# Kernel tuning notes

Measured on AMD Instinct MI355X. Metric: run time of the kernel, lower is better.

Reference implementation:

```python
import jax, jax.numpy as jnp
import numpy as np

B, H, W, C = 8, 64, 64, 256
CB = C // 2          # bottleneck_dim = channels // 2
COMPRESSION = 2      # max-pool factor on flattened spatial axis of phi and g


def setup_inputs() -> dict:
    key = jax.random.key(0)
    k = jax.random.split(key, 5)
    he = lambda kk, fan_in, shape: jax.random.normal(kk, shape, jnp.float32) * np.sqrt(2.0 / fan_in)
    return {
        "x": jax.random.normal(k[0], (B, H, W, C), jnp.float32),
        "W_theta": he(k[1], C, (C, CB)),
        "W_phi": he(k[2], C, (C, CB)),
        "W_g": he(k[3], C, (C, CB)),
        "W_out": he(k[4], CB, (CB, C)),
    }


def _maxpool1d(t, pool):
    # MaxPool1D(pool) along axis 1 of [B, N, C] (valid padding, stride=pool)
    b, n, c = t.shape
    return t.reshape(b, n // pool, pool, c).max(axis=2)


def reference(x, W_theta, W_phi, W_g, W_out):
    b, h, w, c = x.shape
    n = h * w
    xf = x.reshape(b, n, c)                      # flatten spatial dims
    theta = xf @ W_theta                         # [B, N, Cb] (1x1 conv, no bias)
    phi = _maxpool1d(xf @ W_phi, COMPRESSION)    # [B, N/2, Cb]
    g = _maxpool1d(xf @ W_g, COMPRESSION)        # [B, N/2, Cb]
    f = jax.nn.softmax(jnp.einsum('bnd,bmd->bnm', theta, phi), axis=-1)  # [B, N, N/2]
    y = jnp.einsum('bnm,bmd->bnd', f, g)         # [B, N, Cb]
    y = (y @ W_out).reshape(b, h, w, c)          # expand conv back to C
    return x + y                                 # add_residual=True
```

## Files before the change

### kernel.cpp

```cpp
#include <hip/hip_runtime.h>
#include <math.h>

#define BB 8
#define NN 4096
#define MM 2048
#define CC 256
#define CBD 128

typedef __attribute__((ext_vector_type(8))) short s16x8;
typedef __attribute__((ext_vector_type(4))) float f32x4;
typedef __attribute__((ext_vector_type(16))) float f32x16;
typedef unsigned short u16;
typedef unsigned int u32;

__device__ __forceinline__ u16 f2bf(float f) {
    union { float f; u32 u; } v; v.f = f;
    u32 r = v.u + 0x7fffu + ((v.u >> 16) & 1u);
    return (u16)(r >> 16);
}
__device__ __forceinline__ float bf2f(u16 h) {
    union { u32 u; float f; } v; v.u = ((u32)h) << 16; return v.f;
}
__device__ __forceinline__ u32 asu(float f) {
    union { float f; u32 u; } v; v.f = f; return v.u;
}
__device__ __forceinline__ u32 pkbf(float lo, float hi) {
    return __builtin_amdgcn_perm(asu(hi), asu(lo), 0x07060302u);
}

#define MFMA(a, b, c)   __builtin_amdgcn_mfma_f32_16x16x32_bf16(a, b, c, 0, 0, 0)
#define MFMA32(a, b, c) __builtin_amdgcn_mfma_f32_32x32x16_bf16(a, b, c, 0, 0, 0)

__device__ __forceinline__ void gload_lds16(const u16* g, u16* l) {
    __builtin_amdgcn_global_load_lds(
        (const __attribute__((address_space(1))) void*)g,
        (__attribute__((address_space(3))) void*)l, 16, 0, 0);
}

__global__ __launch_bounds__(256) void k_split_w(
    const float* __restrict__ wt, const float* __restrict__ wp,
    const float* __restrict__ wg, const float* __restrict__ wo,
    u16* wth, u16* wtl, u16* wph, u16* wpl, u16* wgh, u16* wgl, u16* wot) {
    int e = blockIdx.x * 256 + threadIdx.x;
    int m = blockIdx.y;
    if (m < 3) {
        const float* src = m == 0 ? wt : (m == 1 ? wp : wg);
        u16* oh = m == 0 ? wth : (m == 1 ? wph : wgh);
        u16* ol = m == 0 ? wtl : (m == 1 ? wpl : wgl);
        int r = e >> 7, c = e & 127;
        float f = src[e];
        u16 hi = f2bf(f);
        oh[c * 256 + r] = hi;
        ol[c * 256 + r] = f2bf(f - bf2f(hi));
    } else {
        int r = e >> 8, c = e & 255;
        wot[c * 128 + r] = f2bf(wo[e]);
    }
}

__global__ __launch_bounds__(256) void k_proj(
    const float* __restrict__ x,
    const u16* __restrict__ wth, const u16* __restrict__ wtl,
    const u16* __restrict__ wph, const u16* __restrict__ wpl,
    const u16* __restrict__ wgh,
    u16* __restrict__ th, u16* __restrict__ tl,
    u16* __restrict__ ph, u16* __restrict__ pl, u16* __restrict__ gt) {
    __shared__ u16 S[31232];
    const int THH = 0, THL = 8704, PHH = 17408, PHL = 21760, GL = 26112;
    u16* sxh = S;
    u16* sxl = S + 2560;
    u16* sw  = S + 5120;
    int tid = threadIdx.x;
    int w = tid >> 6, lane = tid & 63, q = lane >> 4, li = lane & 15;
    int r0 = blockIdx.x * 64;
    int wr2 = (w >> 1) * 32, wcc = (w & 1) * 64;
    const u16* Ws[5] = {wth, wtl, wph, wpl, wgh};

    f32x4 aT[2][4], aP[2][4], aG[2][4];
#pragma unroll
    for (int i = 0; i < 2; i++)
#pragma unroll
        for (int j = 0; j < 4; j++) {
            aT[i][j] = (f32x4)0.f; aP[i][j] = (f32x4)0.f; aG[i][j] = (f32x4)0.f;
        }

    for (int kc = 0; kc < 8; kc++) {
        {
            int row = tid >> 2, seg = tid & 3;
            const float* xp = &x[(size_t)(r0 + row) * 256 + kc * 32 + seg * 8];
            float4 v0 = ((const float4*)xp)[0];
            float4 v1 = ((const float4*)xp)[1];
            float vv[8] = {v0.x, v0.y, v0.z, v0.w, v1.x, v1.y, v1.z, v1.w};
            u16 hh[8], ll[8];
#pragma unroll
            for (int t = 0; t < 8; t++) {
                hh[t] = f2bf(vv[t]);
                ll[t] = f2bf(vv[t] - bf2f(hh[t]));
            }
            *(s16x8*)&sxh[row * 40 + seg * 8] = *(s16x8*)&hh[0];
            *(s16x8*)&sxl[row * 40 + seg * 8] = *(s16x8*)&ll[0];
        }
#pragma unroll
        for (int u = 0; u < 10; u++) {
            int mat = u >> 1;
            int col = (u & 1) * 64 + (tid >> 2), ch = tid & 3;
            s16x8 v = *(const s16x8*)&Ws[mat][(size_t)col * 256 + kc * 32 + ch * 8];
            *(s16x8*)&sw[mat * 5120 + col * 40 + ch * 8] = v;
        }
        __syncthreads();

        s16x8 ah[2], al[2];
#pragma unroll
        for (int i = 0; i < 2; i++) {
            ah[i] = *(const s16x8*)&sxh[(wr2 + i * 16 + li) * 40 + q * 8];
            al[i] = *(const s16x8*)&sxl[(wr2 + i * 16 + li) * 40 + q * 8];
        }
#pragma unroll
        for (int j = 0; j < 4; j++) {
            int col = wcc + j * 16 + li;
            s16x8 bth = *(const s16x8*)&sw[0 * 5120 + col * 40 + q * 8];
            s16x8 btl = *(const s16x8*)&sw[1 * 5120 + col * 40 + q * 8];
            s16x8 bph = *(const s16x8*)&sw[2 * 5120 + col * 40 + q * 8];
            s16x8 bpl = *(const s16x8*)&sw[3 * 5120 + col * 40 + q * 8];
            s16x8 bgh = *(const s16x8*)&sw[4 * 5120 + col * 40 + q * 8];
#pragma unroll
            for (int i = 0; i < 2; i++) {
                aT[i][j] = MFMA(ah[i], bth, aT[i][j]);
                aT[i][j] = MFMA(al[i], bth, aT[i][j]);
                aT[i][j] = MFMA(ah[i], btl, aT[i][j]);
                aP[i][j] = MFMA(ah[i], bph, aP[i][j]);
                aP[i][j] = MFMA(al[i], bph, aP[i][j]);
                aP[i][j] = MFMA(ah[i], bpl, aP[i][j]);
                aG[i][j] = MFMA(ah[i], bgh, aG[i][j]);
                aG[i][j] = MFMA(al[i], bgh, aG[i][j]);
            }
        }
        __syncthreads();
    }

#pragma unroll
    for (int i = 0; i < 2; i++)
#pragma unroll
        for (int j = 0; j < 4; j++) {
            int col = wcc + j * 16 + li;
#pragma unroll
            for (int reg = 0; reg < 4; reg++) {
                int row = wr2 + i * 16 + q * 4 + reg;
                float v = aT[i][j][reg];
                u16 hi = f2bf(v);
                S[THH + row * 136 + col] = hi;
                S[THL + row * 136 + col] = f2bf(v - bf2f(hi));
            }
#pragma unroll
            for (int pr = 0; pr < 2; pr++) {
                int ml = (wr2 >> 1) + i * 8 + q * 2 + pr;
                float vp = fmaxf(aP[i][j][pr * 2], aP[i][j][pr * 2 + 1]);
                u16 hi = f2bf(vp);
                S[PHH + ml * 136 + col] = hi;
                S[PHL + ml * 136 + col] = f2bf(vp - bf2f(hi));
                float vg = fmaxf(aG[i][j][pr * 2], aG[i][j][pr * 2 + 1]);
                int ml2 = (ml & ~12) | ((ml & 4) << 1) | ((ml & 8) >> 1);
                S[GL + col * 40 + ml2] = f2bf(vg);
            }
        }
    __syncthreads();

#pragma unroll
    for (int p2 = 0; p2 < 4; p2++) {
        int u2 = tid + p2 * 256;
        int row = u2 >> 4, chk = u2 & 15;
        size_t gb = (size_t)(r0 + row) * 128 + chk * 8;
        *(s16x8*)&th[gb] = *(const s16x8*)&S[THH + row * 136 + chk * 8];
        *(s16x8*)&tl[gb] = *(const s16x8*)&S[THL + row * 136 + chk * 8];
    }
    {
        int row = tid >> 3, chk = tid & 7;
        size_t gb = (size_t)((r0 >> 1) + row) * 128 + chk * 16;
        *(s16x8*)&ph[gb]     = *(const s16x8*)&S[PHH + row * 136 + chk * 16];
        *(s16x8*)&ph[gb + 8] = *(const s16x8*)&S[PHH + row * 136 + chk * 16 + 8];
        *(s16x8*)&pl[gb]     = *(const s16x8*)&S[PHL + row * 136 + chk * 16];
        *(s16x8*)&pl[gb + 8] = *(const s16x8*)&S[PHL + row * 136 + chk * 16 + 8];
    }
    {
        int col = tid >> 1, half = tid & 1;
        int b = r0 >> 12;
        int base = (r0 >> 1) & 2047;
        size_t gb = (size_t)b * (128 * 2048) + (size_t)col * 2048 + base + half * 16;
        *(s16x8*)&gt[gb]     = *(const s16x8*)&S[GL + col * 40 + half * 16];
        *(s16x8*)&gt[gb + 8] = *(const s16x8*)&S[GL + col * 40 + half * 16 + 8];
    }
}

__global__ __launch_bounds__(256, 2) void k_attn(
    const u16* __restrict__ th, const u16* __restrict__ tl,
    const u16* __restrict__ ph, const u16* __restrict__ pl,
    const u16* __restrict__ gt, u16* __restrict__ ot,
    float* __restrict__ Mv, float* __restrict__ Lv) {
    __shared__ u16 smem[24576];
    u16* skh = smem;
    u16* skl = smem + 8192;
    u16* sg  = smem + 16384;
    int tid = threadIdx.x, w = tid >> 6, lane = tid & 63;
    int q = lane & 31, b = lane >> 5;
    int bb = blockIdx.y;
    int s = blockIdx.x & 1;
    int qt = blockIdx.x >> 1;
    int n0 = qt * 128;
    int row128 = w * 32 + q;
    size_t qrow = ((size_t)bb * 4096 + n0 + row128) * 128;

    s16x8 Qh[8], Ql[8];
#pragma unroll
    for (int ks = 0; ks < 8; ks++) {
        Qh[ks] = *(const s16x8*)&th[qrow + ks * 16 + b * 8];
        Ql[ks] = *(const s16x8*)&tl[qrow + ks * 16 + b * 8];
    }
    float mrow = -INFINITY, lrow = 0.f;
    f32x16 o[4];
#pragma unroll
    for (int c = 0; c < 4; c++) o[c] = (f32x16)0.f;

    int r_hi = lane >> 4, c_hi = lane & 15;
    int r_lo = lane >> 3, c_lo = lane & 7;
    int k0 = s * 1024;

    for (int kt = 0; kt < 16; kt++) {
        int m0 = k0 + kt * 64;
        if (kt) __syncthreads();
#pragma unroll
        for (int jj = 0; jj < 4; jj++) {
            int r = w * 16 + jj * 4 + r_hi;
            int gc = c_hi ^ (r & 7);
            size_t ga = (((size_t)(bb * 2048 + m0 + r)) << 7) + gc * 8;
            gload_lds16(&ph[ga], &skh[(w * 16 + jj * 4) << 7]);
            gload_lds16(&pl[ga], &skl[(w * 16 + jj * 4) << 7]);
            int r2 = w * 32 + jj * 8 + r_lo;
            int gc2 = c_lo ^ (r2 & 7);
            size_t ga2 = (size_t)bb * (128 * 2048) + (size_t)r2 * 2048 + m0 + gc2 * 8;
            gload_lds16(&gt[ga2], &sg[(w * 32 + jj * 8) << 6]);
        }
        __syncthreads();

        f32x16 S[2];
        S[0] = (f32x16)0.f; S[1] = (f32x16)0.f;
        __builtin_amdgcn_s_setprio(1);
#pragma unroll
        for (int ks = 0; ks < 8; ks++) {
            int off0 = (q << 7) + (((ks * 2 + b) ^ (q & 7)) << 3);
            int r1 = 32 + q;
            int off1 = (r1 << 7) + (((ks * 2 + b) ^ (r1 & 7)) << 3);
            s16x8 ah0 = *(const s16x8*)&skh[off0];
            s16x8 al0 = *(const s16x8*)&skl[off0];
            s16x8 ah1 = *(const s16x8*)&skh[off1];
            s16x8 al1 = *(const s16x8*)&skl[off1];
            S[0] = MFMA32(ah0, Qh[ks], S[0]);
            S[1] = MFMA32(ah1, Qh[ks], S[1]);
            S[0] = MFMA32(al0, Qh[ks], S[0]);
            S[1] = MFMA32(al1, Qh[ks], S[1]);
            S[0] = MFMA32(ah0, Ql[ks], S[0]);
            S[1] = MFMA32(ah1, Ql[ks], S[1]);
        }
        __builtin_amdgcn_s_setprio(0);

        float t0[8];
#pragma unroll
        for (int r = 0; r < 8; r++)
            t0[r] = fmaxf(fmaxf(S[0][r], S[0][r + 8]),
                          fmaxf(S[1][r], S[1][r + 8]));
        float u0 = fmaxf(t0[0], t0[1]), u1 = fmaxf(t0[2], t0[3]);
        float u2 = fmaxf(t0[4], t0[5]), u3 = fmaxf(t0[6], t0[7]);
        float vmax = fmaxf(fmaxf(u0, u1), fmaxf(u2, u3));
        vmax = fmaxf(vmax, __shfl_xor(vmax, 32, 64));

        if (!__all(vmax - mrow <= 20.f)) {
            float nm = fmaxf(mrow, vmax);
            float alph = __expf(mrow - nm);
            mrow = nm;
            lrow *= alph;
#pragma unroll
            for (int c = 0; c < 4; c++)
#pragma unroll
                for (int r = 0; r < 16; r++) o[c][r] *= alph;
        }
        float rs0 = 0.f, rs1 = 0.f, rs2 = 0.f, rs3 = 0.f;
#pragma unroll
        for (int r = 0; r < 4; r++) {
            float p00 = __expf(S[0][r] - mrow);      S[0][r] = p00;      rs0 += p00;
            float p01 = __expf(S[0][r + 4] - mrow);  S[0][r + 4] = p01;  rs1 += p01;
            float p02 = __expf(S[0][r + 8] - mrow);  S[0][r + 8] = p02;  rs2 += p02;
            float p03 = __expf(S[0][r + 12] - mrow); S[0][r + 12] = p03; rs3 += p03;
            float p10 = __expf(S[1][r] - mrow);      S[1][r] = p10;      rs0 += p10;
            float p11 = __expf(S[1][r + 4] - mrow);  S[1][r + 4] = p11;  rs1 += p11;
            float p12 = __expf(S[1][r + 8] - mrow);  S[1][r + 8] = p12;  rs2 += p12;
            float p13 = __expf(S[1][r + 12] - mrow); S[1][r + 12] = p13; rs3 += p13;
        }
        float rs = (rs0 + rs1) + (rs2 + rs3);
        rs += __shfl_xor(rs, 32, 64);
        lrow += rs;

        __builtin_amdgcn_s_setprio(1);
#pragma unroll
        for (int t = 0; t < 4; t++) {
            int half = t >> 1, base = (t & 1) * 8;
            s16x8 Pf;
            u32* pf = (u32*)&Pf;
#pragma unroll
            for (int r2 = 0; r2 < 4; r2++)
                pf[r2] = pkbf(S[half][base + 2 * r2], S[half][base + 2 * r2 + 1]);
#pragma unroll
            for (int c = 0; c < 4; c++) {
                int ch = c * 32 + q;
                int off = (ch << 6) + (((t * 2 + b) ^ (ch & 7)) << 3);
                s16x8 gv = *(const s16x8*)&sg[off];
                o[c] = MFMA32(gv, Pf, o[c]);
            }
        }
        __builtin_amdgcn_s_setprio(0);
    }
    __syncthreads();

    u16* sc = smem;
#pragma unroll
    for (int c = 0; c < 4; c++)
#pragma unroll
        for (int r2 = 0; r2 < 8; r2++) {
            int ch = c * 32 + ((r2 & 1) << 1) + 8 * (r2 >> 1) + 4 * b;
            u32 pk = (u32)f2bf(o[c][2 * r2]) | ((u32)f2bf(o[c][2 * r2 + 1]) << 16);
            *(u32*)&sc[row128 * 136 + ch] = pk;
        }
    __syncthreads();
    size_t obase = ((size_t)s * 32768 + (size_t)bb * 4096 + n0) * 128;
    int rowy = tid >> 1;
#pragma unroll
    for (int j = 0; j < 8; j++) {
        int chk = (tid & 1) * 8 + j;
        s16x8 v = *(const s16x8*)&sc[rowy * 136 + chk * 8];
        *(s16x8*)&ot[obase + (size_t)rowy * 128 + chk * 8] = v;
    }
    if (b == 0) {
        int gi = s * 32768 + bb * 4096 + n0 + row128;
        Mv[gi] = mrow;
        Lv[gi] = lrow;
    }
}

__global__ __launch_bounds__(256) void k_out(
    const u16* __restrict__ ot, const float* __restrict__ Mv,
    const float* __restrict__ Lv, const u16* __restrict__ wot,
    const float* __restrict__ x, float* __restrict__ out) {
    __shared__ char lds_o[36864];
    u16 (*sy)[72] = (u16(*)[72])lds_o;
    u16 (*sw)[72] = (u16(*)[72])(lds_o + 18432);
    int tid = threadIdx.x, w = tid >> 6, lane = tid & 63, q = lane >> 4, li = lane & 15;
    int r0 = blockIdx.x * 128, c0 = blockIdx.y * 128;
    int wr = (w >> 1) * 64, wc = (w & 1) * 64;
    const size_t OS = (size_t)32768 * 128;

    float a1v[4], a2v[4];
#pragma unroll
    for (int i = 0; i < 4; i++) {
        int gr = r0 + ((tid + i * 256) >> 3);
        float m1 = Mv[gr], m2 = Mv[32768 + gr];
        float l1 = Lv[gr], l2 = Lv[32768 + gr];
        float Mx = fmaxf(m1, m2);
        float e1 = __expf(m1 - Mx), e2 = __expf(m2 - Mx);
        float inv = 1.f / (l1 * e1 + l2 * e2);
        a1v[i] = e1 * inv;
        a2v[i] = e2 * inv;
    }

    f32x4 acc[4][4];
#pragma unroll
    for (int i = 0; i < 4; i++)
#pragma unroll
        for (int j = 0; j < 4; j++) acc[i][j] = (f32x4)0.f;

    for (int kc = 0; kc < 2; kc++) {
#pragma unroll
        for (int i = 0; i < 4; i++) {
            int ch = tid + i * 256;
            int r = ch >> 3, cc = (ch & 7) * 8;
            size_t ga = (size_t)(r0 + r) * 128 + kc * 64 + cc;
            s16x8 o1 = *(const s16x8*)&ot[ga];
            s16x8 o2 = *(const s16x8*)&ot[OS + ga];
            s16x8 yv;
#pragma unroll
            for (int e = 0; e < 8; e++)
                yv[e] = (short)f2bf(bf2f((u16)o1[e]) * a1v[i] +
                                    bf2f((u16)o2[e]) * a2v[i]);
            *(s16x8*)&sy[r][cc] = yv;
            *(s16x8*)&sw[r][cc] = *(const s16x8*)&wot[(size_t)(c0 + r) * 128 + kc * 64 + cc];
        }
        __syncthreads();
#pragma unroll
        for (int ks = 0; ks < 2; ks++)
#pragma unroll
            for (int i = 0; i < 4; i++) {
                s16x8 a = *(const s16x8*)&sy[wr + i * 16 + li][ks * 32 + q * 8];
#pragma unroll
                for (int j = 0; j < 4; j++) {
                    s16x8 bv = *(const s16x8*)&sw[wc + j * 16 + li][ks * 32 + q * 8];
                    acc[i][j] = MFMA(a, bv, acc[i][j]);
                }
            }
        __syncthreads();
    }

    float* sT = (float*)lds_o;
#pragma unroll
    for (int h = 0; h < 2; h++) {
        __syncthreads();
        if ((w >> 1) == h) {
#pragma unroll
            for (int i = 0; i < 4; i++)
#pragma unroll
                for (int j = 0; j < 4; j++)
#pragma unroll
                    for (int reg = 0; reg < 4; reg++)
                        sT[(i * 16 + q * 4 + reg) * 132 + wc + j * 16 + li] =
                            acc[i][j][reg];
        }
        __syncthreads();
#pragma unroll
        for (int p = 0; p < 8; p++) {
            int r = (tid >> 5) + p * 8;
            int c4 = (tid & 31) * 4;
            f32x4 yv = *(f32x4*)&sT[r * 132 + c4];
            size_t row = (size_t)(r0 + h * 64 + r);
            float4 xv = *(const float4*)&x[row * 256 + c0 + c4];
            float4 ov;
            ov.x = xv.x + yv[0]; ov.y = xv.y + yv[1];
            ov.z = xv.z + yv[2]; ov.w = xv.w + yv[3];
            *(float4*)&out[row * 256 + c0 + c4] = ov;
        }
    }
}

extern "C" void kernel_launch(void* const* d_in, const int* in_sizes, int n_in,
                              void* d_out, int out_size, void* d_ws, size_t ws_size,
                              hipStream_t stream) {
    const float* x  = (const float*)d_in[0];
    const float* wt = (const float*)d_in[1];
    const float* wp = (const float*)d_in[2];
    const float* wg = (const float*)d_in[3];
    const float* wo = (const float*)d_in[4];
    float* out = (float*)d_out;

    char* p = (char*)d_ws;
    auto alloc = [&](size_t bytes) {
        char* r = p;
        p += (bytes + 255) & ~(size_t)255;
        return r;
    };
    const size_t NT = (size_t)BB * NN * CBD;
    const size_t NP = (size_t)BB * MM * CBD;

    u16* wth = (u16*)alloc(CC * CBD * 2);
    u16* wtl = (u16*)alloc(CC * CBD * 2);
    u16* wph = (u16*)alloc(CC * CBD * 2);
    u16* wpl = (u16*)alloc(CC * CBD * 2);
    u16* wgh = (u16*)alloc(CC * CBD * 2);
    u16* wgl = (u16*)alloc(CC * CBD * 2);
    u16* wot = (u16*)alloc(CC * CBD * 2);
    u16* th  = (u16*)alloc(NT * 2);
    u16* tl  = (u16*)alloc(NT * 2);
    u16* ph  = (u16*)alloc(NP * 2);
    u16* pl  = (u16*)alloc(NP * 2);
    u16* gt  = (u16*)alloc(NP * 2);
    float* Mv = (float*)alloc(2 * 32768 * 4);
    float* Lv = (float*)alloc(2 * 32768 * 4);
    u16* ot  = (u16*)alloc(2 * NT * 2);

    k_split_w<<<dim3(128, 4), 256, 0, stream>>>(wt, wp, wg, wo,
                                                wth, wtl, wph, wpl, wgh, wgl, wot);
    k_proj<<<dim3(512), 256, 0, stream>>>(x, wth, wtl, wph, wpl, wgh,
                                          th, tl, ph, pl, gt);
    k_attn<<<dim3(64, 8), 256, 0, stream>>>(th, tl, ph, pl, gt, ot, Mv, Lv);
    k_out<<<dim3(256, 2), 256, 0, stream>>>(ot, Mv, Lv, wot, x, out);
}
```

Before: 196.6 us.

## Replace split-bf16 QK^T with single fp16 MFMA and split keys four ways

```diff
diff --git a/kernel.cpp b/kernel.cpp
--- a/kernel.cpp
+++ b/kernel.cpp
@@ -8,6 +8,7 @@
 #define CBD 128
 
 typedef __attribute__((ext_vector_type(8))) short s16x8;
+typedef __attribute__((ext_vector_type(8))) _Float16 f16x8;
 typedef __attribute__((ext_vector_type(4))) float f32x4;
 typedef __attribute__((ext_vector_type(16))) float f32x16;
 typedef unsigned short u16;
@@ -21,6 +22,9 @@
 __device__ __forceinline__ float bf2f(u16 h) {
     union { u32 u; float f; } v; v.u = ((u32)h) << 16; return v.f;
 }
+__device__ __forceinline__ u16 f2h(float f) {
+    union { _Float16 h; u16 u; } v; v.h = (_Float16)f; return v.u;
+}
 __device__ __forceinline__ u32 asu(float f) {
     union { float f; u32 u; } v; v.f = f; return v.u;
 }
@@ -28,8 +32,9 @@
     return __builtin_amdgcn_perm(asu(hi), asu(lo), 0x07060302u);
 }
 
-#define MFMA(a, b, c)   __builtin_amdgcn_mfma_f32_16x16x32_bf16(a, b, c, 0, 0, 0)
-#define MFMA32(a, b, c) __builtin_amdgcn_mfma_f32_32x32x16_bf16(a, b, c, 0, 0, 0)
+#define MFMA(a, b, c)    __builtin_amdgcn_mfma_f32_16x16x32_bf16(a, b, c, 0, 0, 0)
+#define MFMA32(a, b, c)  __builtin_amdgcn_mfma_f32_32x32x16_bf16(a, b, c, 0, 0, 0)
+#define MFMA32F(a, b, c) __builtin_amdgcn_mfma_f32_32x32x16_f16(a, b, c, 0, 0, 0)
 
 __device__ __forceinline__ void gload_lds16(const u16* g, u16* l) {
     __builtin_amdgcn_global_load_lds(
@@ -63,10 +68,9 @@
     const u16* __restrict__ wth, const u16* __restrict__ wtl,
     const u16* __restrict__ wph, const u16* __restrict__ wpl,
     const u16* __restrict__ wgh,
-    u16* __restrict__ th, u16* __restrict__ tl,
-    u16* __restrict__ ph, u16* __restrict__ pl, u16* __restrict__ gt) {
+    u16* __restrict__ th, u16* __restrict__ ph, u16* __restrict__ gt) {
     __shared__ u16 S[31232];
-    const int THH = 0, THL = 8704, PHH = 17408, PHL = 21760, GL = 26112;
+    const int THH = 0, PHH = 17408, GL = 26112;
     u16* sxh = S;
     u16* sxl = S + 2560;
     u16* sw  = S + 5120;
@@ -146,18 +150,13 @@
 #pragma unroll
             for (int reg = 0; reg < 4; reg++) {
                 int row = wr2 + i * 16 + q * 4 + reg;
-                float v = aT[i][j][reg];
-                u16 hi = f2bf(v);
-                S[THH + row * 136 + col] = hi;
-                S[THL + row * 136 + col] = f2bf(v - bf2f(hi));
+                S[THH + row * 136 + col] = f2h(aT[i][j][reg]);
             }
 #pragma unroll
             for (int pr = 0; pr < 2; pr++) {
                 int ml = (wr2 >> 1) + i * 8 + q * 2 + pr;
                 float vp = fmaxf(aP[i][j][pr * 2], aP[i][j][pr * 2 + 1]);
-                u16 hi = f2bf(vp);
-                S[PHH + ml * 136 + col] = hi;
-                S[PHL + ml * 136 + col] = f2bf(vp - bf2f(hi));
+                S[PHH + ml * 136 + col] = f2h(vp);
                 float vg = fmaxf(aG[i][j][pr * 2], aG[i][j][pr * 2 + 1]);
                 int ml2 = (ml & ~12) | ((ml & 4) << 1) | ((ml & 8) >> 1);
                 S[GL + col * 40 + ml2] = f2bf(vg);
@@ -171,15 +170,12 @@
         int row = u2 >> 4, chk = u2 & 15;
         size_t gb = (size_t)(r0 + row) * 128 + chk * 8;
         *(s16x8*)&th[gb] = *(const s16x8*)&S[THH + row * 136 + chk * 8];
-        *(s16x8*)&tl[gb] = *(const s16x8*)&S[THL + row * 136 + chk * 8];
     }
     {
         int row = tid >> 3, chk = tid & 7;
         size_t gb = (size_t)((r0 >> 1) + row) * 128 + chk * 16;
         *(s16x8*)&ph[gb]     = *(const s16x8*)&S[PHH + row * 136 + chk * 16];
         *(s16x8*)&ph[gb + 8] = *(const s16x8*)&S[PHH + row * 136 + chk * 16 + 8];
-        *(s16x8*)&pl[gb]     = *(const s16x8*)&S[PHL + row * 136 + chk * 16];
-        *(s16x8*)&pl[gb + 8] = *(const s16x8*)&S[PHL + row * 136 + chk * 16 + 8];
     }
     {
         int col = tid >> 1, half = tid & 1;
@@ -191,30 +187,27 @@
     }
 }
 
-__global__ __launch_bounds__(256, 2) void k_attn(
-    const u16* __restrict__ th, const u16* __restrict__ tl,
-    const u16* __restrict__ ph, const u16* __restrict__ pl,
+__global__ __launch_bounds__(256, 4) void k_attn(
+    const u16* __restrict__ th, const u16* __restrict__ ph,
     const u16* __restrict__ gt, u16* __restrict__ ot,
     float* __restrict__ Mv, float* __restrict__ Lv) {
-    __shared__ u16 smem[24576];
+    __shared__ u16 smem[17408];
     u16* skh = smem;
-    u16* skl = smem + 8192;
-    u16* sg  = smem + 16384;
+    u16* sg  = smem + 8192;
     int tid = threadIdx.x, w = tid >> 6, lane = tid & 63;
     int q = lane & 31, b = lane >> 5;
     int bb = blockIdx.y;
-    int s = blockIdx.x & 1;
-    int qt = blockIdx.x >> 1;
+    int s = blockIdx.x & 3;
+    int qt = blockIdx.x >> 2;
     int n0 = qt * 128;
     int row128 = w * 32 + q;
     size_t qrow = ((size_t)bb * 4096 + n0 + row128) * 128;
 
-    s16x8 Qh[8], Ql[8];
-#pragma unroll
-    for (int ks = 0; ks < 8; ks++) {
-        Qh[ks] = *(const s16x8*)&th[qrow + ks * 16 + b * 8];
-        Ql[ks] = *(const s16x8*)&tl[qrow + ks * 16 + b * 8];
-    }
+    f16x8 Qf[8];
+#pragma unroll
+    for (int ks = 0; ks < 8; ks++)
+        Qf[ks] = *(const f16x8*)&th[qrow + ks * 16 + b * 8];
+
     float mrow = -INFINITY, lrow = 0.f;
     f32x16 o[4];
 #pragma unroll
@@ -222,9 +215,9 @@
 
     int r_hi = lane >> 4, c_hi = lane & 15;
     int r_lo = lane >> 3, c_lo = lane & 7;
-    int k0 = s * 1024;
-
-    for (int kt = 0; kt < 16; kt++) {
+    int k0 = s * 512;
+
+    for (int kt = 0; kt < 8; kt++) {
         int m0 = k0 + kt * 64;
         if (kt) __syncthreads();
 #pragma unroll
@@ -233,7 +226,6 @@
             int gc = c_hi ^ (r & 7);
             size_t ga = (((size_t)(bb * 2048 + m0 + r)) << 7) + gc * 8;
             gload_lds16(&ph[ga], &skh[(w * 16 + jj * 4) << 7]);
-            gload_lds16(&pl[ga], &skl[(w * 16 + jj * 4) << 7]);
             int r2 = w * 32 + jj * 8 + r_lo;
             int gc2 = c_lo ^ (r2 & 7);
             size_t ga2 = (size_t)bb * (128 * 2048) + (size_t)r2 * 2048 + m0 + gc2 * 8;
@@ -249,16 +241,10 @@
             int off0 = (q << 7) + (((ks * 2 + b) ^ (q & 7)) << 3);
             int r1 = 32 + q;
             int off1 = (r1 << 7) + (((ks * 2 + b) ^ (r1 & 7)) << 3);
-            s16x8 ah0 = *(const s16x8*)&skh[off0];
-            s16x8 al0 = *(const s16x8*)&skl[off0];
-            s16x8 ah1 = *(const s16x8*)&skh[off1];
-            s16x8 al1 = *(const s16x8*)&skl[off1];
-            S[0] = MFMA32(ah0, Qh[ks], S[0]);
-            S[1] = MFMA32(ah1, Qh[ks], S[1]);
-            S[0] = MFMA32(al0, Qh[ks], S[0]);
-            S[1] = MFMA32(al1, Qh[ks], S[1]);
-            S[0] = MFMA32(ah0, Ql[ks], S[0]);
-            S[1] = MFMA32(ah1, Ql[ks], S[1]);
+            f16x8 a0 = *(const f16x8*)&skh[off0];
+            f16x8 a1 = *(const f16x8*)&skh[off1];
+            S[0] = MFMA32F(a0, Qf[ks], S[0]);
+            S[1] = MFMA32F(a1, Qf[ks], S[1]);
         }
         __builtin_amdgcn_s_setprio(0);
 
@@ -356,17 +342,20 @@
     int wr = (w >> 1) * 64, wc = (w & 1) * 64;
     const size_t OS = (size_t)32768 * 128;
 
-    float a1v[4], a2v[4];
+    float av[4][4];
 #pragma unroll
     for (int i = 0; i < 4; i++) {
         int gr = r0 + ((tid + i * 256) >> 3);
-        float m1 = Mv[gr], m2 = Mv[32768 + gr];
-        float l1 = Lv[gr], l2 = Lv[32768 + gr];
-        float Mx = fmaxf(m1, m2);
-        float e1 = __expf(m1 - Mx), e2 = __expf(m2 - Mx);
-        float inv = 1.f / (l1 * e1 + l2 * e2);
-        a1v[i] = e1 * inv;
-        a2v[i] = e2 * inv;
+        float m0 = Mv[gr], m1 = Mv[32768 + gr];
+        float m2 = Mv[65536 + gr], m3 = Mv[98304 + gr];
+        float l0 = Lv[gr], l1 = Lv[32768 + gr];
+        float l2 = Lv[65536 + gr], l3 = Lv[98304 + gr];
+        float Mx = fmaxf(fmaxf(m0, m1), fmaxf(m2, m3));
+        float e0 = __expf(m0 - Mx), e1 = __expf(m1 - Mx);
+        float e2 = __expf(m2 - Mx), e3 = __expf(m3 - Mx);
+        float inv = 1.f / (l0 * e0 + l1 * e1 + l2 * e2 + l3 * e3);
+        av[0][i] = e0 * inv; av[1][i] = e1 * inv;
+        av[2][i] = e2 * inv; av[3][i] = e3 * inv;
     }
 
     f32x4 acc[4][4];
@@ -383,11 +372,15 @@
             size_t ga = (size_t)(r0 + r) * 128 + kc * 64 + cc;
             s16x8 o1 = *(const s16x8*)&ot[ga];
             s16x8 o2 = *(const s16x8*)&ot[OS + ga];
+            s16x8 o3 = *(const s16x8*)&ot[2 * OS + ga];
+            s16x8 o4 = *(const s16x8*)&ot[3 * OS + ga];
             s16x8 yv;
 #pragma unroll
             for (int e = 0; e < 8; e++)
-                yv[e] = (short)f2bf(bf2f((u16)o1[e]) * a1v[i] +
-                                    bf2f((u16)o2[e]) * a2v[i]);
+                yv[e] = (short)f2bf(bf2f((u16)o1[e]) * av[0][i] +
+                                    bf2f((u16)o2[e]) * av[1][i] +
+                                    bf2f((u16)o3[e]) * av[2][i] +
+                                    bf2f((u16)o4[e]) * av[3][i]);
             *(s16x8*)&sy[r][cc] = yv;
             *(s16x8*)&sw[r][cc] = *(const s16x8*)&wot[(size_t)(c0 + r) * 128 + kc * 64 + cc];
         }
@@ -463,18 +456,16 @@
     u16* wgl = (u16*)alloc(CC * CBD * 2);
     u16* wot = (u16*)alloc(CC * CBD * 2);
     u16* th  = (u16*)alloc(NT * 2);
-    u16* tl  = (u16*)alloc(NT * 2);
     u16* ph  = (u16*)alloc(NP * 2);
-    u16* pl  = (u16*)alloc(NP * 2);
     u16* gt  = (u16*)alloc(NP * 2);
-    float* Mv = (float*)alloc(2 * 32768 * 4);
-    float* Lv = (float*)alloc(2 * 32768 * 4);
-    u16* ot  = (u16*)alloc(2 * NT * 2);
+    float* Mv = (float*)alloc(4 * 32768 * 4);
+    float* Lv = (float*)alloc(4 * 32768 * 4);
+    u16* ot  = (u16*)alloc(4 * NT * 2);
 
     k_split_w<<<dim3(128, 4), 256, 0, stream>>>(wt, wp, wg, wo,
                                                 wth, wtl, wph, wpl, wgh, wgl, wot);
     k_proj<<<dim3(512), 256, 0, stream>>>(x, wth, wtl, wph, wpl, wgh,
-                                          th, tl, ph, pl, gt);
-    k_attn<<<dim3(64, 8), 256, 0, stream>>>(th, tl, ph, pl, gt, ot, Mv, Lv);
+                                          th, ph, gt);
+    k_attn<<<dim3(128, 8), 256, 0, stream>>>(th, ph, gt, ot, Mv, Lv);
     k_out<<<dim3(256, 2), 256, 0, stream>>>(ot, Mv, Lv, wot, x, out);
 }
```

New measurement: 244.3 us. 1.24x slower.
